# Kernel tuning notes

Measured on AMD Instinct MI355X. Metric: run time of the kernel, lower is better.

The kernel has to match this reference:

```python
import jax, jax.numpy as jnp
import numpy as np

NUM_HEADS = 4
LOCAL_RADIUS = 2


def setup_inputs() -> dict:
    key = jax.random.key(0)
    ks = jax.random.split(key, 7)
    B, C, H, W = 1, 256, 40, 40
    O = 256  # out_channels
    s = 1.0 / np.sqrt(C).astype(np.float32)
    x = jax.random.normal(ks[0], (B, C, H, W), dtype=jnp.float32)
    Wq = jax.random.normal(ks[1], (C, O), dtype=jnp.float32) * s
    Wk = jax.random.normal(ks[2], (C, O), dtype=jnp.float32) * s
    Wv = jax.random.normal(ks[3], (C, O), dtype=jnp.float32) * s
    bq = jnp.zeros((O,), jnp.float32)
    bk = jnp.zeros((O,), jnp.float32)
    bv = jnp.zeros((O,), jnp.float32)
    return {"x": x, "Wq": Wq, "bq": bq, "Wk": Wk, "bk": bk, "Wv": Wv, "bv": bv}


def reference(x, Wq, bq, Wk, bk, Wv, bv):
    B, C, H, W = x.shape
    N = H * W
    O = Wq.shape[1]
    hd = O // NUM_HEADS
    # Faithful to torch: x.view(B, N, -1) is a raw row-major reshape of (B,C,H,W)
    xf = x.reshape(B, N, C)
    # projections -> (B, heads, N, head_dim)
    q = (xf @ Wq + bq).reshape(B, N, NUM_HEADS, hd).transpose(0, 2, 1, 3)
    k = (xf @ Wk + bk).reshape(B, N, NUM_HEADS, hd).transpose(0, 2, 1, 3)
    v = (xf @ Wv + bv).reshape(B, N, NUM_HEADS, hd).transpose(0, 2, 1, 3)
    scale = jnp.asarray(O, jnp.float32) ** 0.5
    acc = jnp.zeros_like(v)
    # 25 shifted full-attention passes; roll is over (heads, points) axes,
    # exactly matching torch key.roll(shifts=(h,w), dims=(-3,-2)).
    for h in range(-LOCAL_RADIUS, LOCAL_RADIUS + 1):
        for w in range(-LOCAL_RADIUS, LOCAL_RADIUS + 1):
            rk = jnp.roll(k, shift=(h, w), axis=(1, 2))
            scores = jnp.einsum('bhnd,bhmd->bhnm', q, rk) / scale  # (B,h,N,N)
            attn = jax.nn.softmax(scores, axis=-1)
            rv = jnp.roll(v, shift=(-h, -w), axis=(1, 2))
            acc = acc + jnp.einsum('bhnm,bhmd->bhnd', attn, rv)
    # (B, heads, N, hd) -> (B, N, O)
    return acc.transpose(0, 2, 1, 3).reshape(B, N, O)
```

## Files before the change

kernel.cpp:

```cpp
#include <hip/hip_runtime.h>
#include <hip/hip_bf16.h>
#include <stdint.h>

typedef __attribute__((ext_vector_type(8))) __bf16 bf16x8;
typedef __attribute__((ext_vector_type(4))) float f32x4;

#define N_PTS 1600
#define HD    64

#define OFF_WT   0u
#define OFF_BIAS 393216u
#define OFF_VHT  394752u
#define OFF_QH   1213952u
#define OFF_KF   2033152u
#define OFF_VF   2852352u

__device__ __forceinline__ float bf2f(ushort h) {
  union { uint32_t u; float f; } v; v.u = ((uint32_t)h) << 16; return v.f;
}
__device__ __forceinline__ ushort f2bf(float f) {
  union { float f; uint32_t u; } v; v.f = f;
  uint32_t u = v.u;
  return (ushort)((u + 0x7FFFu + ((u >> 16) & 1u)) >> 16);
}
__device__ __forceinline__ uint32_t pk2(float a, float b) {
  union { __hip_bfloat162 h; uint32_t u; } cv;
  cv.h = __float22bfloat162_rn(make_float2(a, b));
  return cv.u;
}

__device__ __forceinline__ int detect_f32(const ushort* xu, int* shflag) {
  int t = threadIdx.x & 255;
  if (t == 0) *shflag = 0;
  __syncthreads();
  int local = 0;
#pragma unroll
  for (int i = 0; i < 4; ++i) {
    float v = bf2f(xu[(t * 4 + i) * 2]);
    if (!(fabsf(v) < 1e4f)) local = 1;
  }
  if (local) atomicOr(shflag, 1);
  __syncthreads();
  return *shflag;
}

__global__ void k_prep(const void* __restrict__ x, const void* __restrict__ Wq,
                       const void* __restrict__ bq, const void* __restrict__ Wk,
                       const void* __restrict__ bk, const void* __restrict__ Wv,
                       const void* __restrict__ bv, char* __restrict__ ws) {
  __shared__ int shflag;
  __shared__ ushort tileb[32][33];
  int isf32 = detect_f32((const ushort*)x, &shflag);
  int b = blockIdx.x, t = threadIdx.x;

  if (b < 192) {
    int z = b >> 6, tile = b & 63;
    const void* W = (z == 0) ? Wq : ((z == 1) ? Wk : Wv);
    int o0 = (tile & 7) * 32, k0 = (tile >> 3) * 32;
    int tx = t & 31, ty = t >> 5;
#pragma unroll
    for (int i = 0; i < 32; i += 8) {
      int kk = (k0 + ty + i) * 256 + o0 + tx;
      tileb[ty + i][tx] = isf32 ? f2bf(((const float*)W)[kk]) : ((const ushort*)W)[kk];
    }
    __syncthreads();
    ushort* WT = (ushort*)(ws + OFF_WT) + z * 65536;
#pragma unroll
    for (int i = 0; i < 32; i += 8)
      WT[(o0 + ty + i) * 256 + k0 + tx] = tileb[tx][ty + i];
  } else {
    ushort* bb = (ushort*)(ws + OFF_BIAS);
#pragma unroll
    for (int z = 0; z < 3; ++z) {
      const void* B = (z == 0) ? bq : ((z == 1) ? bk : bv);
      bb[z * 256 + t] = isf32 ? f2bf(((const float*)B)[t]) : ((const ushort*)B)[t];
    }
  }
}

__launch_bounds__(512)
__global__ void k_proj(const void* __restrict__ x, const ushort* __restrict__ WT,
                       const ushort* __restrict__ bias3, char* __restrict__ ws) {
  __shared__ int shflag;
  __shared__ ushort ktile[2][4][16][72];
  int isf32 = detect_f32((const ushort*)x, &shflag);
  int tid = threadIdx.x;
  int half = tid >> 8;
  int job = blockIdx.x + 150 * half;
  int z = job / 100, nb = job % 100;
  int n0 = nb * 16;
  const ushort* WTz = WT + z * 65536;
  const ushort* bias = bias3 + z * 256;
  int t256 = tid & 255;
  int head = t256 >> 6, lane = t256 & 63;
  int c = lane & 15, quad = lane >> 4;

  f32x4 acc[4];
#pragma unroll
  for (int i = 0; i < 4; ++i) acc[i] = (f32x4){0.f, 0.f, 0.f, 0.f};

  int ebase = (n0 + c) * 256;
#pragma unroll
  for (int kt = 0; kt < 8; ++kt) {
    bf16x8 a;
    if (isf32) {
      const float4* X4 = (const float4*)x;
      int i4 = (ebase + kt * 32 + quad * 8) >> 2;
      float4 f0 = X4[i4], f1 = X4[i4 + 1];
      union { ushort us[8]; bf16x8 v; } cv;
      cv.us[0] = f2bf(f0.x); cv.us[1] = f2bf(f0.y);
      cv.us[2] = f2bf(f0.z); cv.us[3] = f2bf(f0.w);
      cv.us[4] = f2bf(f1.x); cv.us[5] = f2bf(f1.y);
      cv.us[6] = f2bf(f1.z); cv.us[7] = f2bf(f1.w);
      a = cv.v;
    } else {
      a = *(const bf16x8*)((const ushort*)x + ebase + kt * 32 + quad * 8);
    }
#pragma unroll
    for (int os = 0; os < 4; ++os) {
      bf16x8 bfr = *(const bf16x8*)(WTz + (head * 64 + os * 16 + c) * 256 + kt * 32 + quad * 8);
      acc[os] = __builtin_amdgcn_mfma_f32_16x16x32_bf16(a, bfr, acc[os], 0, 0, 0);
    }
  }

  float scale = (z == 0) ? 0.0625f * 1.44269504088896f : 1.0f;
  if (z != 2) {
#pragma unroll
    for (int os = 0; os < 4; ++os) {
      float bval = bf2f(bias[head * 64 + os * 16 + c]);
#pragma unroll
      for (int r = 0; r < 4; ++r)
        ktile[half][head][quad * 4 + r][os * 16 + c] = f2bf((acc[os][r] + bval) * scale);
    }
  } else {
    ushort* VhT = (ushort*)(ws + OFF_VHT);
#pragma unroll
    for (int os = 0; os < 4; ++os) {
      int row = head * 64 + os * 16 + c;
      float bval = bf2f(bias[row]);
      ushort4 v;
      v.x = f2bf(acc[os][0] + bval); v.y = f2bf(acc[os][1] + bval);
      v.z = f2bf(acc[os][2] + bval); v.w = f2bf(acc[os][3] + bval);
      *(ushort4*)(VhT + (size_t)row * N_PTS + n0 + quad * 4) = v;
    }
  }
  __syncthreads();

  if (z == 0) {
    ushort* Qh = (ushort*)(ws + OFF_QH);
    int kl = lane >> 2, d0 = (lane & 3) * 16;
    bf16x8 v0 = *(const bf16x8*)&ktile[half][head][kl][d0];
    bf16x8 v1 = *(const bf16x8*)&ktile[half][head][kl][d0 + 8];
    ushort* qrow = Qh + (size_t)head * (N_PTS * HD) + (size_t)(n0 + kl) * HD + d0;
    *(bf16x8*)qrow = v0;
    *(bf16x8*)(qrow + 8) = v1;
  } else if (z == 1) {
    ushort* Kf = (ushort*)(ws + OFF_KF);
    int hf = nb & 1, t = nb >> 1;
    int quad_o = lane >> 4, chp = (lane >> 3) & 1, cc = (lane & 7) + hf * 8;
#pragma unroll
    for (int e = 0; e < 2; ++e) {
      int ch = chp + 2 * e;
      int kl = ((cc >> 2) << 3) + (cc & 3) + ((ch >> 1) << 2) - hf * 16;
      int d0 = (ch & 1) * 32 + quad_o * 8;
      bf16x8 v = *(const bf16x8*)&ktile[half][head][kl][d0];
      *(bf16x8*)(Kf + ((((size_t)head * 50 + t) * 4 + ch) * 64 + quad_o * 16 + cc) * 8) = v;
    }
  }
}

__global__ void k_fragV(const ushort* __restrict__ VhT, ushort* __restrict__ Vf) {
  int idx = blockIdx.x * 512 + threadIdx.x;
  int lane = idx & 63, ch = (idx >> 6) & 3;
  int rest = idx >> 8;
  int t = rest % 50, g = rest / 50;
  int c = lane & 15, quad = lane >> 4;
  int d = ch * 16 + c;
  int m0 = t * 32 + quad * 8;
  const ushort* row = VhT + (size_t)(g * HD + d) * N_PTS;
  int mp = (m0 == 0) ? 1592 : m0 - 8;
  int mn = (m0 == 1592) ? 0 : m0 + 8;
  union { bf16x8 v[3]; ushort us[24]; } w;
  w.v[0] = *(const bf16x8*)(row + mp);
  w.v[1] = *(const bf16x8*)(row + m0);
  w.v[2] = *(const bf16x8*)(row + mn);
  union { ushort us[8]; bf16x8 v; } o;
#pragma unroll
  for (int j = 0; j < 8; ++j) {
    float s = bf2f(w.us[4 + j]) + bf2f(w.us[6 + j]) + bf2f(w.us[8 + j]) +
              bf2f(w.us[10 + j]) + bf2f(w.us[12 + j]);
    o.us[j] = f2bf(s);
  }
  *(bf16x8*)(Vf + (size_t)idx * 8) = o.v;
}

__device__ __forceinline__ bf16x8 pack_p8(const f32x4& s0, const f32x4& s1, float& lp) {
  float e0 = exp2f(s0[0]), e1 = exp2f(s0[1]), e2 = exp2f(s0[2]), e3 = exp2f(s0[3]);
  float e4 = exp2f(s1[0]), e5 = exp2f(s1[1]), e6 = exp2f(s1[2]), e7 = exp2f(s1[3]);
  lp += ((e0 + e1) + (e2 + e3)) + ((e4 + e5) + (e6 + e7));
  union { uint32_t u[4]; bf16x8 v; } r;
  r.u[0] = pk2(e0, e1); r.u[1] = pk2(e2, e3);
  r.u[2] = pk2(e4, e5); r.u[3] = pk2(e6, e7);
  return r.v;
}

#define MFMA16(a, b, cc) __builtin_amdgcn_mfma_f32_16x16x32_bf16(a, b, cc, 0, 0, 0)

#define LOADT(sfx, t) do {                                            \
    const char* kt_ = kfp + (size_t)(t) * 4096;                       \
    const char* vt_ = vfp + (size_t)(t) * 4096;                       \
    ka0##sfx = *(const bf16x8*)(kt_);                                 \
    ka1##sfx = *(const bf16x8*)(kt_ + 1024);                          \
    kb0##sfx = *(const bf16x8*)(kt_ + 2048);                          \
    kb1##sfx = *(const bf16x8*)(kt_ + 3072);                          \
    vb0##sfx = *(const bf16x8*)(vt_);                                 \
    vb1##sfx = *(const bf16x8*)(vt_ + 1024);                          \
    vb2##sfx = *(const bf16x8*)(vt_ + 2048);                          \
    vb3##sfx = *(const bf16x8*)(vt_ + 3072);                          \
  } while (0)

#define COMPUTE(sfx) do {                                             \
    __builtin_amdgcn_s_setprio(1);                                    \
    f32x4 s0 = MFMA16(ka0##sfx, qa00, z4);                            \
    s0 = MFMA16(ka1##sfx, qa01, s0);                                  \
    f32x4 s1 = MFMA16(kb0##sfx, qa00, z4);                            \
    s1 = MFMA16(kb1##sfx, qa01, s1);                                  \
    bf16x8 pa0 = pack_p8(s0, s1, lp0);                                \
    oacc0[0] = MFMA16(pa0, vb0##sfx, oacc0[0]);                       \
    oacc0[1] = MFMA16(pa0, vb1##sfx, oacc0[1]);                       \
    oacc0[2] = MFMA16(pa0, vb2##sfx, oacc0[2]);                       \
    oacc0[3] = MFMA16(pa0, vb3##sfx, oacc0[3]);                       \
    s0 = MFMA16(ka0##sfx, qa10, z4);                                  \
    s0 = MFMA16(ka1##sfx, qa11, s0);                                  \
    s1 = MFMA16(kb0##sfx, qa10, z4);                                  \
    s1 = MFMA16(kb1##sfx, qa11, s1);                                  \
    bf16x8 pa1 = pack_p8(s0, s1, lp1);                                \
    oacc1[0] = MFMA16(pa1, vb0##sfx, oacc1[0]);                       \
    oacc1[1] = MFMA16(pa1, vb1##sfx, oacc1[1]);                       \
    oacc1[2] = MFMA16(pa1, vb2##sfx, oacc1[2]);                       \
    oacc1[3] = MFMA16(pa1, vb3##sfx, oacc1[3]);                       \
    __builtin_amdgcn_s_setprio(0);                                    \
  } while (0)

__launch_bounds__(512)
__global__ void k_attn(const ushort* __restrict__ Qh, const ushort* __restrict__ Kf,
                       const ushort* __restrict__ Vf, const void* __restrict__ x,
                       void* __restrict__ out) {
  __shared__ int shflag;
  __shared__ float obuf[8][16][68];
  __shared__ float lbuf[8][16];
  int isf32 = detect_f32((const ushort*)x, &shflag);

  int qt = blockIdx.x;
  int hp = blockIdx.y;
  int tid = threadIdx.x, sp = tid >> 6, lane = tid & 63;
  int kg = sp & 3, zh = sp >> 2;
  int vg = (2 * hp - kg + 8) & 3;
  int c = lane & 15, quad = lane >> 4;
  int n0 = qt * 16;

  const ushort* q0row = Qh + ((hp    ) * N_PTS + n0 + c) * HD;
  const ushort* q1row = Qh + ((hp + 2) * N_PTS + n0 + c) * HD;
  bf16x8 qa00 = *(const bf16x8*)(q0row + quad * 8);
  bf16x8 qa01 = *(const bf16x8*)(q0row + 32 + quad * 8);
  bf16x8 qa10 = *(const bf16x8*)(q1row + quad * 8);
  bf16x8 qa11 = *(const bf16x8*)(q1row + 32 + quad * 8);

  f32x4 oacc0[4], oacc1[4];
#pragma unroll
  for (int i = 0; i < 4; ++i) {
    oacc0[i] = (f32x4){0.f, 0.f, 0.f, 0.f};
    oacc1[i] = (f32x4){0.f, 0.f, 0.f, 0.f};
  }
  float lp0 = 0.f, lp1 = 0.f;

  int off = zh * 25;
  const int iters = 25;
  const f32x4 z4 = (f32x4){0.f, 0.f, 0.f, 0.f};

  const char* kfp = (const char*)Kf + (size_t)(kg * 50 + off) * 4096 + lane * 16;
  const char* vfp = (const char*)Vf + (size_t)(vg * 50 + off) * 4096 + lane * 16;

  bf16x8 ka0A, ka1A, kb0A, kb1A, vb0A, vb1A, vb2A, vb3A;
  bf16x8 ka0B, ka1B, kb0B, kb1B, vb0B, vb1B, vb2B, vb3B;

  LOADT(A, 0);
  int it = 0;
  for (; it + 2 <= iters; it += 2) {
    LOADT(B, it + 1);
    COMPUTE(A);
    int tn = (it + 2 < iters) ? (it + 2) : (it + 1);
    LOADT(A, tn);
    COMPUTE(B);
  }
  if (it < iters) COMPUTE(A);

  lp0 += __shfl_xor(lp0, 16, 64); lp0 += __shfl_xor(lp0, 32, 64);
  lp1 += __shfl_xor(lp1, 16, 64); lp1 += __shfl_xor(lp1, 32, 64);

#pragma unroll
  for (int h = 0; h < 2; ++h) {
    __syncthreads();
    const f32x4* oa = h ? oacc1 : oacc0;
#pragma unroll
    for (int ds = 0; ds < 4; ++ds)
#pragma unroll
      for (int r = 0; r < 4; ++r)
        obuf[sp][quad * 4 + r][ds * 16 + c] = oa[ds][r];
    if (quad == 0) lbuf[sp][c] = h ? lp1 : lp0;
    __syncthreads();

    int q = tid >> 5, dp = (tid & 31) * 2;
    int hq = hp + 2 * h;
    float a0 = 0.f, a1 = 0.f;
#pragma unroll
    for (int g = 0; g < 4; ++g) {
      float n0v = obuf[g][q][dp]     + obuf[g + 4][q][dp];
      float n1v = obuf[g][q][dp + 1] + obuf[g + 4][q][dp + 1];
      float l   = lbuf[g][q] + lbuf[g + 4][q];
      float w   = (g == ((hq + 2) & 3)) ? 2.f : 1.f;
      float rl  = w / l;
      a0 += n0v * rl; a1 += n1v * rl;
    }
    size_t oidx = (size_t)(n0 + q) * 256 + hq * 64 + dp;
    if (isf32) {
      ((float2*)out)[oidx >> 1] = make_float2(a0, a1);
    } else {
      ((uint32_t*)out)[oidx >> 1] = pk2(a0, a1);
    }
  }
}

extern "C" void kernel_launch(void* const* d_in, const int* in_sizes, int n_in,
                              void* d_out, int out_size, void* d_ws, size_t ws_size,
                              hipStream_t stream) {
  char* ws = (char*)d_ws;
  ushort* WT    = (ushort*)(ws + OFF_WT);
  ushort* bias3 = (ushort*)(ws + OFF_BIAS);
  ushort* VhT   = (ushort*)(ws + OFF_VHT);
  ushort* Qh    = (ushort*)(ws + OFF_QH);
  ushort* Kf    = (ushort*)(ws + OFF_KF);
  ushort* Vf    = (ushort*)(ws + OFF_VF);

  k_prep<<<193, 256, 0, stream>>>(d_in[0], d_in[1], d_in[2], d_in[3],
                                  d_in[4], d_in[5], d_in[6], ws);
  k_proj<<<150, 512, 0, stream>>>(d_in[0], WT, bias3, ws);
  k_fragV<<<100, 512, 0, stream>>>(VhT, Vf);
  k_attn<<<dim3(100, 2), 512, 0, stream>>>(Qh, Kf, Vf, d_in[0], d_out);
}
```

Baseline: 110.4 us.

## Sum shifted x rows before V projection and drop the fragV kernel

Linearity lets the 5-tap rolled sum over V be applied to the input rows before projection instead of after. The prep kernel now builds a summed-x buffer from rows n-4..n+4, and the projection scales the V bias by 5. The projection then writes V directly in MFMA fragment layout, which removes the separate fragV kernel launch and the VhT intermediate. The costs are extra prep blocks that read x five times, and bf16 rounding of the summed input before the matmul, which changes numerics slightly.

```diff
diff --git a/kernel.cpp b/kernel.cpp
--- a/kernel.cpp
+++ b/kernel.cpp
@@ -10,7 +10,7 @@
 
 #define OFF_WT   0u
 #define OFF_BIAS 393216u
-#define OFF_VHT  394752u
+#define OFF_XS   394752u
 #define OFF_QH   1213952u
 #define OFF_KF   2033152u
 #define OFF_VF   2852352u
@@ -68,13 +68,47 @@
 #pragma unroll
     for (int i = 0; i < 32; i += 8)
       WT[(o0 + ty + i) * 256 + k0 + tx] = tileb[tx][ty + i];
-  } else {
+  } else if (b == 192) {
     ushort* bb = (ushort*)(ws + OFF_BIAS);
 #pragma unroll
     for (int z = 0; z < 3; ++z) {
       const void* B = (z == 0) ? bq : ((z == 1) ? bk : bv);
       bb[z * 256 + t] = isf32 ? f2bf(((const float*)B)[t]) : ((const ushort*)B)[t];
     }
+  } else {
+    int jid = (b - 193) * 256 + t;
+    int n = jid >> 5, ch0 = (jid & 31) * 8;
+    int nm4 = n - 4 + ((n < 4) ? 1600 : 0);
+    int nm2 = n - 2 + ((n < 2) ? 1600 : 0);
+    int np2 = n + 2 - ((n >= 1598) ? 1600 : 0);
+    int np4 = n + 4 - ((n >= 1596) ? 1600 : 0);
+    int rows[5] = {nm4, nm2, n, np2, np4};
+    union { ushort us[8]; bf16x8 v; } rv[5];
+    if (isf32) {
+      const float4* X4 = (const float4*)x;
+#pragma unroll
+      for (int r = 0; r < 5; ++r) {
+        int i4 = (rows[r] * 256 + ch0) >> 2;
+        float4 f0 = X4[i4], f1 = X4[i4 + 1];
+        rv[r].us[0] = f2bf(f0.x); rv[r].us[1] = f2bf(f0.y);
+        rv[r].us[2] = f2bf(f0.z); rv[r].us[3] = f2bf(f0.w);
+        rv[r].us[4] = f2bf(f1.x); rv[r].us[5] = f2bf(f1.y);
+        rv[r].us[6] = f2bf(f1.z); rv[r].us[7] = f2bf(f1.w);
+      }
+    } else {
+      const ushort* Xu = (const ushort*)x;
+#pragma unroll
+      for (int r = 0; r < 5; ++r)
+        rv[r].v = *(const bf16x8*)(Xu + rows[r] * 256 + ch0);
+    }
+    union { ushort us[8]; bf16x8 v; } o;
+#pragma unroll
+    for (int j = 0; j < 8; ++j) {
+      float s = bf2f(rv[0].us[j]) + bf2f(rv[1].us[j]) + bf2f(rv[2].us[j]) +
+                bf2f(rv[3].us[j]) + bf2f(rv[4].us[j]);
+      o.us[j] = f2bf(s);
+    }
+    *(bf16x8*)((ushort*)(ws + OFF_XS) + n * 256 + ch0) = o.v;
   }
 }
 
@@ -100,10 +134,13 @@
   for (int i = 0; i < 4; ++i) acc[i] = (f32x4){0.f, 0.f, 0.f, 0.f};
 
   int ebase = (n0 + c) * 256;
+  const ushort* Xs = (const ushort*)(ws + OFF_XS);
 #pragma unroll
   for (int kt = 0; kt < 8; ++kt) {
     bf16x8 a;
-    if (isf32) {
+    if (z == 2) {
+      a = *(const bf16x8*)(Xs + ebase + kt * 32 + quad * 8);
+    } else if (isf32) {
       const float4* X4 = (const float4*)x;
       int i4 = (ebase + kt * 32 + quad * 8) >> 2;
       float4 f0 = X4[i4], f1 = X4[i4 + 1];
@@ -124,25 +161,14 @@
   }
 
   float scale = (z == 0) ? 0.0625f * 1.44269504088896f : 1.0f;
-  if (z != 2) {
-#pragma unroll
-    for (int os = 0; os < 4; ++os) {
-      float bval = bf2f(bias[head * 64 + os * 16 + c]);
-#pragma unroll
-      for (int r = 0; r < 4; ++r)
-        ktile[half][head][quad * 4 + r][os * 16 + c] = f2bf((acc[os][r] + bval) * scale);
-    }
-  } else {
-    ushort* VhT = (ushort*)(ws + OFF_VHT);
-#pragma unroll
-    for (int os = 0; os < 4; ++os) {
-      int row = head * 64 + os * 16 + c;
-      float bval = bf2f(bias[row]);
-      ushort4 v;
-      v.x = f2bf(acc[os][0] + bval); v.y = f2bf(acc[os][1] + bval);
-      v.z = f2bf(acc[os][2] + bval); v.w = f2bf(acc[os][3] + bval);
-      *(ushort4*)(VhT + (size_t)row * N_PTS + n0 + quad * 4) = v;
-    }
+  float bmul = (z == 2) ? 5.f : 1.f;
+#pragma unroll
+  for (int os = 0; os < 4; ++os) {
+    float bval = bf2f(bias[head * 64 + os * 16 + c]);
+#pragma unroll
+    for (int r = 0; r < 4; ++r)
+      ktile[half][head][quad * 4 + r][os * 16 + c] =
+          f2bf((acc[os][r] + bmul * bval) * scale);
   }
   __syncthreads();
 
@@ -166,32 +192,20 @@
       bf16x8 v = *(const bf16x8*)&ktile[half][head][kl][d0];
       *(bf16x8*)(Kf + ((((size_t)head * 50 + t) * 4 + ch) * 64 + quad_o * 16 + cc) * 8) = v;
     }
-  }
-}
-
-__global__ void k_fragV(const ushort* __restrict__ VhT, ushort* __restrict__ Vf) {
-  int idx = blockIdx.x * 512 + threadIdx.x;
-  int lane = idx & 63, ch = (idx >> 6) & 3;
-  int rest = idx >> 8;
-  int t = rest % 50, g = rest / 50;
-  int c = lane & 15, quad = lane >> 4;
-  int d = ch * 16 + c;
-  int m0 = t * 32 + quad * 8;
-  const ushort* row = VhT + (size_t)(g * HD + d) * N_PTS;
-  int mp = (m0 == 0) ? 1592 : m0 - 8;
-  int mn = (m0 == 1592) ? 0 : m0 + 8;
-  union { bf16x8 v[3]; ushort us[24]; } w;
-  w.v[0] = *(const bf16x8*)(row + mp);
-  w.v[1] = *(const bf16x8*)(row + m0);
-  w.v[2] = *(const bf16x8*)(row + mn);
-  union { ushort us[8]; bf16x8 v; } o;
-#pragma unroll
-  for (int j = 0; j < 8; ++j) {
-    float s = bf2f(w.us[4 + j]) + bf2f(w.us[6 + j]) + bf2f(w.us[8 + j]) +
-              bf2f(w.us[10 + j]) + bf2f(w.us[12 + j]);
-    o.us[j] = f2bf(s);
-  }
-  *(bf16x8*)(Vf + (size_t)idx * 8) = o.v;
+  } else {
+    ushort* Vf = (ushort*)(ws + OFF_VF);
+    int hf = nb & 1, t = nb >> 1;
+    int cc = lane & 15, qh = (lane >> 4) & 1, dsp = lane >> 5;
+#pragma unroll
+    for (int e = 0; e < 2; ++e) {
+      int ds = dsp * 2 + e;
+      union { ushort us[8]; bf16x8 v; } o;
+#pragma unroll
+      for (int j = 0; j < 8; ++j)
+        o.us[j] = ktile[half][head][8 * qh + j][ds * 16 + cc];
+      *(bf16x8*)(Vf + ((((size_t)head * 50 + t) * 4 + ds) * 64 + (2 * hf + qh) * 16 + cc) * 8) = o.v;
+    }
+  }
 }
 
 __device__ __forceinline__ bf16x8 pack_p8(const f32x4& s0, const f32x4& s1, float& lp) {
@@ -337,14 +351,12 @@
   char* ws = (char*)d_ws;
   ushort* WT    = (ushort*)(ws + OFF_WT);
   ushort* bias3 = (ushort*)(ws + OFF_BIAS);
-  ushort* VhT   = (ushort*)(ws + OFF_VHT);
   ushort* Qh    = (ushort*)(ws + OFF_QH);
   ushort* Kf    = (ushort*)(ws + OFF_KF);
   ushort* Vf    = (ushort*)(ws + OFF_VF);
 
-  k_prep<<<193, 256, 0, stream>>>(d_in[0], d_in[1], d_in[2], d_in[3],
+  k_prep<<<393, 256, 0, stream>>>(d_in[0], d_in[1], d_in[2], d_in[3],
                                   d_in[4], d_in[5], d_in[6], ws);
   k_proj<<<150, 512, 0, stream>>>(d_in[0], WT, bias3, ws);
-  k_fragV<<<100, 512, 0, stream>>>(VhT, Vf);
   k_attn<<<dim3(100, 2), 512, 0, stream>>>(Qh, Kf, Vf, d_in[0], d_out);
 }
```

Result: faster. 106.5 us, median of 2 (-3.5%).
